# Kernel tuning notes

Measured on AMD Instinct MI355X. Metric: run time of the kernel, lower is better.

## Reference

```python
import jax, jax.numpy as jnp
import numpy as np

D_MODEL = 512
D_ATTN = 128


def setup_inputs() -> dict:
    key = jax.random.key(0)
    k1, k2, k3, k4, k5 = jax.random.split(key, 5)
    B, N = 4, 4096
    x = jax.random.normal(k1, (B, N, D_MODEL), dtype=jnp.float32)
    key_mask = jnp.ones((B, N, 1), dtype=jnp.float32)
    # nn.Linear params (stored as [in, out] for x @ W)
    W_qkv = jax.random.normal(k2, (D_MODEL, 3 * D_ATTN), dtype=jnp.float32) / np.sqrt(D_MODEL)
    b_qkv = jax.random.normal(k3, (3 * D_ATTN,), dtype=jnp.float32) * 0.01
    W_out = jax.random.normal(k4, (D_ATTN, D_MODEL), dtype=jnp.float32) / np.sqrt(D_ATTN)
    b_out = jax.random.normal(k5, (D_MODEL,), dtype=jnp.float32) * 0.01
    return {"x": x, "key_mask": key_mask, "W_qkv": W_qkv, "b_qkv": b_qkv,
            "W_out": W_out, "b_out": b_out}


def reference(x, key_mask, W_qkv, b_qkv, W_out, b_out):
    # Fused QKV projection: [B, N, 3*d_attn]
    qkv = jnp.einsum('bnd,de->bne', x, W_qkv) + b_qkv
    q, k, v = jnp.split(qkv, 3, axis=-1)  # each [B, N, d_attn]
    d_attn = q.shape[-1]
    scale = 1.0 / np.sqrt(d_attn)
    # Full [B, N, N] score matrix (faithful to original einsum)
    scores = jnp.einsum('bnd,bmd->bnm', q, k)
    # Causal mask applied BEFORE scaling (as in original: mask, then *scale)
    N = x.shape[1]
    causal = jnp.tril(jnp.ones((N, N), dtype=bool))  # True = keep
    scores = jnp.where(causal[None, :, :], scores, -jnp.inf)
    scores = scores * scale
    attn = jax.nn.softmax(scores, axis=-1)  # dropout is identity in eval
    out = jnp.einsum('bnm,bmd->bnd', attn, v)
    out = out * key_mask  # broadcast [B, N, 1]
    out = jnp.einsum('bnd,de->bne', out, W_out) + b_out
    return out
```

## Files before the change

### kernel.cpp

```cpp
#include <hip/hip_runtime.h>
#include <hip/hip_bf16.h>
#include <math.h>

typedef __attribute__((ext_vector_type(4))) float f32x4;
typedef __attribute__((ext_vector_type(4))) float fvec4;
typedef __attribute__((ext_vector_type(8))) short bf16x8_t;
typedef __attribute__((ext_vector_type(4))) short bf16x4_t;

static constexpr int BATCH = 4;
static constexpr int SEQ = 4096;
static constexpr int DM = 512;
static constexpr int DA = 128;
static constexpr int BN = BATCH * SEQ;
static constexpr int IPB = 187;
static constexpr int N_ITEMS = BATCH * IPB;

static constexpr float MASKV = -3.0e38f;
static constexpr float MINIT = -1.0e30f;

static __device__ __forceinline__ unsigned short f2bf(float f) {
  unsigned u = __builtin_bit_cast(unsigned, f);
  u += 0x7fffu + ((u >> 16) & 1u);
  return (unsigned short)(u >> 16);
}
static __device__ __forceinline__ float bf2f(unsigned short u) {
  return __builtin_bit_cast(float, ((unsigned)u) << 16);
}
static __device__ __forceinline__ float fexp2(float x) {
#if __has_builtin(__builtin_amdgcn_exp2f)
  return __builtin_amdgcn_exp2f(x);
#else
  return exp2f(x);
#endif
}
static __device__ __forceinline__ unsigned pkbf(float lo, float hi) {
  unsigned r;
  asm("v_cvt_pk_bf16_f32 %0, %1, %2" : "=v"(r) : "v"(lo), "v"(hi));
  return r;
}

#define GLDS16(gsrc, ldst)                                                        \
  __builtin_amdgcn_global_load_lds(                                               \
      (const __attribute__((address_space(1))) void*)(gsrc),                      \
      (__attribute__((address_space(3))) void*)(ldst), 16, 0, 0)

static constexpr float QSC = 0.08838834764831845f * 1.4426950408889634f;

__global__ __launch_bounds__(256) void prep_kernel(
    const float* __restrict__ x, const float* __restrict__ Wqkv,
    const float* __restrict__ Wout, unsigned short* __restrict__ xbf,
    unsigned short* __restrict__ WqT, unsigned short* __restrict__ WoT) {
  long long i = ((long long)blockIdx.x * 256 + threadIdx.x) * 8;
  if (i < (long long)BN * DM) {
    fvec4 a = *(const fvec4*)&x[i];
    fvec4 b = *(const fvec4*)&x[i + 4];
    union { bf16x8_t v; unsigned short u[8]; } pk;
    pk.u[0] = f2bf(a[0]); pk.u[1] = f2bf(a[1]); pk.u[2] = f2bf(a[2]); pk.u[3] = f2bf(a[3]);
    pk.u[4] = f2bf(b[0]); pk.u[5] = f2bf(b[1]); pk.u[6] = f2bf(b[2]); pk.u[7] = f2bf(b[3]);
    *(bf16x8_t*)&xbf[i] = pk.v;
  }
  int t = blockIdx.x * 256 + threadIdx.x;
  if (t < 512 * 384) {
    int k = t / 384, n = t - k * 384;
    WqT[n * 512 + k] = f2bf(Wqkv[t]);
  }
  if (t < 128 * 512) {
    int k = t >> 9, n = t & 511;
    WoT[n * 128 + k] = f2bf(Wout[t]);
  }
}

__global__ __launch_bounds__(512, 4) void qkv_kernel(
    const unsigned short* __restrict__ xbf, const unsigned short* __restrict__ WqT,
    const float* __restrict__ bias, unsigned short* __restrict__ qbf,
    unsigned short* __restrict__ kpk, unsigned short* __restrict__ vpk) {
  __shared__ unsigned short Alds[128 * 64];
  __shared__ unsigned short Blds[128 * 64];

  const int m0 = blockIdx.x * 128;
  const int n0 = blockIdx.y * 128;
  const int tid = threadIdx.x;
  const int wave = tid >> 6, lane = tid & 63;
  const int g = lane >> 4, lr = lane & 15;
  const int wm = wave >> 2, wn = wave & 3;

  const int srow = lane >> 3;
  const int sslot = lane & 7;
  const int sksw = ((sslot ^ srow) * 8);

  f32x4 acc[4][2] = {};

  for (int kb = 0; kb < DM; kb += 64) {
    __syncthreads();
#pragma unroll
    for (int i = 0; i < 2; ++i) {
      int ch = wave * 2 + i;
      GLDS16(&xbf[(size_t)(m0 + ch * 8 + srow) * DM + kb + sksw],
             (char*)Alds + ch * 1024);
      GLDS16(&WqT[(size_t)(n0 + ch * 8 + srow) * DM + kb + sksw],
             (char*)Blds + ch * 1024);
    }
    asm volatile("s_waitcnt vmcnt(0)" ::: "memory");
    __syncthreads();

#pragma unroll
    for (int c2 = 0; c2 < 2; ++c2) {
      bf16x8_t ar[4], br[2];
#pragma unroll
      for (int mi = 0; mi < 4; ++mi) {
        int row = wm * 64 + mi * 16 + lr;
        ar[mi] = *(const bf16x8_t*)&Alds[row * 64 + (((c2 * 4 + g) ^ (row & 7)) * 8)];
      }
#pragma unroll
      for (int ni = 0; ni < 2; ++ni) {
        int row = wn * 32 + ni * 16 + lr;
        br[ni] = *(const bf16x8_t*)&Blds[row * 64 + (((c2 * 4 + g) ^ (row & 7)) * 8)];
      }
#pragma unroll
      for (int mi = 0; mi < 4; ++mi)
#pragma unroll
        for (int ni = 0; ni < 2; ++ni)
          acc[mi][ni] = __builtin_amdgcn_mfma_f32_16x16x32_bf16(ar[mi], br[ni],
                                                                acc[mi][ni], 0, 0, 0);
    }
  }

  if (n0 == 0) {
#pragma unroll
    for (int ni = 0; ni < 2; ++ni) {
      int col = wn * 32 + ni * 16 + lr;
      float bv = bias[col];
#pragma unroll
      for (int mi = 0; mi < 4; ++mi) {
        int tokb = m0 + wm * 64 + mi * 16 + 4 * g;
#pragma unroll
        for (int r = 0; r < 4; ++r)
          qbf[(size_t)(tokb + r) * DA + col] = f2bf((acc[mi][ni][r] + bv) * QSC);
      }
    }
  } else if (n0 == 128) {
#pragma unroll
    for (int ni = 0; ni < 2; ++ni) {
      int kd = wn * 32 + ni * 16 + lr;
      float bv = bias[128 + kd];
      int unit = (kd >> 5) * 4 + ((kd >> 3) & 3);
      int elem = kd & 7;
#pragma unroll
      for (int mi = 0; mi < 4; ++mi) {
        int tokb = m0 + wm * 64 + mi * 16 + 4 * g;
#pragma unroll
        for (int r = 0; r < 4; ++r) {
          int token = tokb + r;
          int tile32 = token >> 5;
          int u = (((token >> 4) & 1) * 16) + unit;
          kpk[(size_t)tile32 * 4096 + u * 128 + (token & 15) * 8 + elem] =
              f2bf(acc[mi][ni][r] + bv);
        }
      }
    }
  } else {
#pragma unroll
    for (int mi = 0; mi < 4; ++mi) {
      int keyb = m0 + wm * 64 + mi * 16 + 4 * g;
      int tile32 = keyb >> 5;
      int kl0 = keyb & 31;
      int gp = (kl0 >> 2) & 3;
      int jhi = kl0 >> 4;
#pragma unroll
      for (int ni = 0; ni < 2; ++ni) {
        int d = wn * 32 + ni * 16 + lr;
        float bv = bias[256 + d];
        union { bf16x4_t v; unsigned short u[4]; } pk;
#pragma unroll
        for (int r = 0; r < 4; ++r) pk.u[r] = f2bf(acc[mi][ni][r] + bv);
        int unit = (d >> 4) * 4 + gp;
        *(bf16x4_t*)&vpk[(size_t)tile32 * 4096 + unit * 128 + (d & 15) * 8 + jhi * 4] =
            pk.v;
      }
    }
  }
}

static __device__ __forceinline__ void softmax64(
    f32x4 s[4], float& m_r, float& l_r, f32x4* oacc, bf16x8_t pb[2]) {
  float tmax = MASKV;
#pragma unroll
  for (int ct = 0; ct < 4; ++ct)
#pragma unroll
    for (int r = 0; r < 4; ++r) tmax = fmaxf(tmax, s[ct][r]);
  tmax = fmaxf(tmax, __shfl_xor(tmax, 16, 64));
  tmax = fmaxf(tmax, __shfl_xor(tmax, 32, 64));
  if (!__all(tmax <= m_r + 10.0f)) {
    float mn = fmaxf(m_r, tmax);
    float al = fexp2(m_r - mn);
    m_r = mn;
    l_r *= al;
#pragma unroll
    for (int t = 0; t < 8; ++t)
#pragma unroll
      for (int r = 0; r < 4; ++r) oacc[t][r] *= al;
  }
  float rs = 0.f;
#pragma unroll
  for (int ct = 0; ct < 4; ++ct)
#pragma unroll
    for (int r = 0; r < 4; ++r) {
      float p = fexp2(s[ct][r] - m_r);
      s[ct][r] = p;
      rs += p;
    }
  rs += __shfl_xor(rs, 16, 64);
  rs += __shfl_xor(rs, 32, 64);
  l_r += rs;
#pragma unroll
  for (int h = 0; h < 2; ++h) {
    union { unsigned u[4]; bf16x8_t v; } pk;
    pk.u[0] = pkbf(s[2 * h][0], s[2 * h][1]);
    pk.u[1] = pkbf(s[2 * h][2], s[2 * h][3]);
    pk.u[2] = pkbf(s[2 * h + 1][0], s[2 * h + 1][1]);
    pk.u[3] = pkbf(s[2 * h + 1][2], s[2 * h + 1][3]);
    pb[h] = pk.v;
  }
}

__global__ __launch_bounds__(256, 3) void attn_kernel(
    const unsigned short* __restrict__ qbf, const unsigned short* __restrict__ kpk,
    const unsigned short* __restrict__ vpk, const float* __restrict__ key_mask,
    unsigned short* __restrict__ part_o, float* __restrict__ part_ml,
    unsigned short* __restrict__ ctx) {
  __shared__ unsigned short Klds[2][8192];
  __shared__ unsigned short Vlds[8192];

  const int flat = blockIdx.x;
  const int b = flat & 3;
  const int idxr = flat >> 2;
  int rem = idxr;
  int qb = 31;
  for (;;) {
    int nc = (qb + 3) / 3;
    if (rem < nc) break;
    rem -= nc;
    --qb;
  }
  const int ci = rem;
  const bool direct = (qb < 3);
  const int key0 = ci * 384;
  const int nkeys = min(384, (qb + 1) * 128 - key0);
  const int nt = nkeys >> 6;

  const int tid = threadIdx.x;
  const int wave = tid >> 6, lane = tid & 63;
  const int g = lane >> 4, lr = lane & 15;
  const int q0 = wave * 16 + lr;
  const int q1 = q0 + 64;

  bf16x8_t qf0[4], qf1[4];
  {
    const unsigned short* qbase = qbf + ((size_t)(b * SEQ + qb * 128)) * DA + g * 8;
#pragma unroll
    for (int c = 0; c < 4; ++c) {
      qf0[c] = *(const bf16x8_t*)(qbase + (size_t)q0 * DA + c * 32);
      qf1[c] = *(const bf16x8_t*)(qbase + (size_t)q1 * DA + c * 32);
    }
  }

  f32x4 oacc0[8] = {}, oacc1[8] = {};
  float m0r = MINIT, l0 = 0.f, m1r = MINIT, l1 = 0.f;

  const int t32b = b * 128 + ci * 12;
  const unsigned short* ksrc = kpk + (size_t)t32b * 4096 + wave * 2048 + lane * 8;
  const unsigned short* vsrc = vpk + (size_t)t32b * 4096 + wave * 2048 + lane * 8;

#define STAGEK(buf, tt)                                                      \
  do {                                                                       \
    char* kd_ = (char*)Klds[buf] + wave * 4096;                              \
    _Pragma("unroll")                                                        \
    for (int i_ = 0; i_ < 4; ++i_)                                           \
      GLDS16(ksrc + (size_t)(tt) * 8192 + i_ * 512, kd_ + i_ * 1024);        \
  } while (0)
#define STAGEV(tt)                                                           \
  do {                                                                       \
    char* vd_ = (char*)Vlds + wave * 4096;                                   \
    _Pragma("unroll")                                                        \
    for (int i_ = 0; i_ < 4; ++i_)                                           \
      GLDS16(vsrc + (size_t)(tt) * 8192 + i_ * 512, vd_ + i_ * 1024);        \
  } while (0)

  STAGEK(0, 0);

  for (int tt = 0; tt < nt; ++tt) {
    const int cur = tt & 1;
    STAGEV(tt);
    if (tt + 1 < nt) {
      STAGEK(cur ^ 1, tt + 1);
      asm volatile("s_waitcnt vmcnt(8)" ::: "memory");
    } else {
      asm volatile("s_waitcnt vmcnt(4)" ::: "memory");
    }
    __builtin_amdgcn_s_barrier();
    __builtin_amdgcn_sched_barrier(0);

    f32x4 s0[4] = {}, s1[4] = {};
    __builtin_amdgcn_s_setprio(1);
#pragma unroll
    for (int ct = 0; ct < 4; ++ct)
#pragma unroll
      for (int c = 0; c < 4; ++c) {
        bf16x8_t kf = *(const bf16x8_t*)&Klds[cur][(ct >> 1) * 4096 +
                                                   (((ct & 1) * 16 + c * 4 + g) * 16 + lr) * 8];
        s0[ct] = __builtin_amdgcn_mfma_f32_16x16x32_bf16(kf, qf0[c], s0[ct], 0, 0, 0);
        s1[ct] = __builtin_amdgcn_mfma_f32_16x16x32_bf16(kf, qf1[c], s1[ct], 0, 0, 0);
      }
    __builtin_amdgcn_s_setprio(0);

    const int koff = key0 + tt * 64 - qb * 128;
    if (koff + 63 > wave * 16) {
      int thr = q0 - koff;
#pragma unroll
      for (int ct = 0; ct < 4; ++ct)
#pragma unroll
        for (int r = 0; r < 4; ++r)
          if (16 * ct + 4 * g + r > thr) s0[ct][r] = MASKV;
    }
    if (koff + 63 > 64 + wave * 16) {
      int thr = q1 - koff;
#pragma unroll
      for (int ct = 0; ct < 4; ++ct)
#pragma unroll
        for (int r = 0; r < 4; ++r)
          if (16 * ct + 4 * g + r > thr) s1[ct][r] = MASKV;
    }

    bf16x8_t pb0[2], pb1[2];
    softmax64(s0, m0r, l0, oacc0, pb0);
    softmax64(s1, m1r, l1, oacc1, pb1);

    if (tt + 1 < nt) {
      asm volatile("s_waitcnt vmcnt(4)" ::: "memory");
    } else {
      asm volatile("s_waitcnt vmcnt(0)" ::: "memory");
    }
    __builtin_amdgcn_s_barrier();
    __builtin_amdgcn_sched_barrier(0);

    __builtin_amdgcn_s_setprio(1);
#pragma unroll
    for (int t = 0; t < 8; ++t)
#pragma unroll
      for (int h = 0; h < 2; ++h) {
        bf16x8_t vf = *(const bf16x8_t*)&Vlds[h * 4096 + ((t * 4 + g) * 16 + lr) * 8];
        oacc0[t] = __builtin_amdgcn_mfma_f32_16x16x32_bf16(vf, pb0[h], oacc0[t], 0, 0, 0);
        oacc1[t] = __builtin_amdgcn_mfma_f32_16x16x32_bf16(vf, pb1[h], oacc1[t], 0, 0, 0);
      }
    __builtin_amdgcn_s_setprio(0);

    __builtin_amdgcn_s_barrier();
  }
#undef STAGEK
#undef STAGEV

  const int slot = b * IPB + idxr;
#pragma unroll
  for (int grp = 0; grp < 2; ++grp) {
    const int row = grp ? q1 : q0;
    const f32x4* oa = grp ? oacc1 : oacc0;
    const float mr = grp ? m1r : m0r;
    const float lr_ = grp ? l1 : l0;
    if (direct) {
      float km = key_mask[b * SEQ + qb * 128 + row];
      float inv = km / lr_;
      unsigned short* co = ctx + ((size_t)(b * SEQ + qb * 128 + row)) * DA;
#pragma unroll
      for (int t = 0; t < 8; ++t) {
        union { bf16x4_t v; unsigned short u[4]; } pk;
#pragma unroll
        for (int r = 0; r < 4; ++r) pk.u[r] = f2bf(oa[t][r] * inv);
        *(bf16x4_t*)&co[t * 16 + 4 * g] = pk.v;
      }
    } else {
      unsigned short* po = part_o + (size_t)slot * 16384 + (size_t)row * 128;
#pragma unroll
      for (int t = 0; t < 8; ++t) {
        union { bf16x4_t v; unsigned short u[4]; } pk;
#pragma unroll
        for (int r = 0; r < 4; ++r) pk.u[r] = f2bf(oa[t][r]);
        *(bf16x4_t*)&po[t * 16 + 4 * g] = pk.v;
      }
      if (g == 0) {
        float2 ml = make_float2(mr, lr_);
        *(float2*)&part_ml[((size_t)slot * 128 + row) * 2] = ml;
      }
    }
  }
}

__global__ __launch_bounds__(512) void combine_kernel(
    const unsigned short* __restrict__ part_o, const float* __restrict__ part_ml,
    const float* __restrict__ key_mask, unsigned short* __restrict__ ctx) {
  const int qb = 3 + (blockIdx.x >> 2);
  const int rq = blockIdx.x & 3;
  const int b = blockIdx.y;
  const int nc = (qb + 3) / 3;
  int idx0 = 0;
  for (int q = 31; q > qb; --q) idx0 += (q + 3) / 3;
  const int row = rq * 32 + (threadIdx.x >> 4);
  const int cs = threadIdx.x & 15;

  float m = MINIT;
  for (int ci = 0; ci < nc; ++ci) {
    int slot = b * IPB + idx0 + ci;
    m = fmaxf(m, part_ml[((size_t)slot * 128 + row) * 2 + 0]);
  }
  float l = 0.f;
  float acc[8];
#pragma unroll
  for (int k = 0; k < 8; ++k) acc[k] = 0.f;
  for (int ci = 0; ci < nc; ++ci) {
    int slot = b * IPB + idx0 + ci;
    float mi = part_ml[((size_t)slot * 128 + row) * 2 + 0];
    float li = part_ml[((size_t)slot * 128 + row) * 2 + 1];
    float w = fexp2(mi - m);
    l += w * li;
    const unsigned short* po =
        part_o + (size_t)slot * 16384 + (size_t)row * 128 + cs * 8;
    bf16x8_t v = *(const bf16x8_t*)po;
#pragma unroll
    for (int jj = 0; jj < 8; ++jj) acc[jj] += w * bf2f((unsigned short)v[jj]);
  }
  int rowg = b * SEQ + qb * 128 + row;
  float sc = key_mask[rowg] / l;
  union { bf16x8_t v; unsigned short u[8]; } pk;
#pragma unroll
  for (int jj = 0; jj < 8; ++jj) pk.u[jj] = f2bf(acc[jj] * sc);
  *(bf16x8_t*)&ctx[(size_t)rowg * 128 + cs * 8] = pk.v;
}

__global__ __launch_bounds__(512, 4) void outproj_kernel(
    const unsigned short* __restrict__ ctx, const unsigned short* __restrict__ WoT,
    const float* __restrict__ bias, float* __restrict__ out) {
  __shared__ unsigned short Alds[128 * 64];
  __shared__ unsigned short Blds[128 * 64];

  const int m0 = blockIdx.x * 128;
  const int n0 = blockIdx.y * 128;
  const int tid = threadIdx.x;
  const int wave = tid >> 6, lane = tid & 63;
  const int g = lane >> 4, lr = lane & 15;
  const int wm = wave >> 2, wn = wave & 3;

  const int srow = lane >> 3;
  const int sslot = lane & 7;
  const int sksw = ((sslot ^ srow) * 8);

  f32x4 acc[4][2] = {};

  for (int kb = 0; kb < DA; kb += 64) {
    __syncthreads();
#pragma unroll
    for (int i = 0; i < 2; ++i) {
      int ch = wave * 2 + i;
      GLDS16(&ctx[(size_t)(m0 + ch * 8 + srow) * DA + kb + sksw],
             (char*)Alds + ch * 1024);
      GLDS16(&WoT[(size_t)(n0 + ch * 8 + srow) * DA + kb + sksw],
             (char*)Blds + ch * 1024);
    }
    asm volatile("s_waitcnt vmcnt(0)" ::: "memory");
    __syncthreads();

#pragma unroll
    for (int c2 = 0; c2 < 2; ++c2) {
      bf16x8_t ar[4], br[2];
#pragma unroll
      for (int mi = 0; mi < 4; ++mi) {
        int row = wm * 64 + mi * 16 + lr;
        ar[mi] = *(const bf16x8_t*)&Alds[row * 64 + (((c2 * 4 + g) ^ (row & 7)) * 8)];
      }
#pragma unroll
      for (int ni = 0; ni < 2; ++ni) {
        int row = wn * 32 + ni * 16 + lr;
        br[ni] = *(const bf16x8_t*)&Blds[row * 64 + (((c2 * 4 + g) ^ (row & 7)) * 8)];
      }
#pragma unroll
      for (int mi = 0; mi < 4; ++mi)
#pragma unroll
        for (int ni = 0; ni < 2; ++ni)
          acc[mi][ni] = __builtin_amdgcn_mfma_f32_16x16x32_bf16(ar[mi], br[ni],
                                                                acc[mi][ni], 0, 0, 0);
    }
  }

#pragma unroll
  for (int ni = 0; ni < 2; ++ni) {
    int col = n0 + wn * 32 + ni * 16 + lr;
    float bv = bias[col];
#pragma unroll
    for (int mi = 0; mi < 4; ++mi) {
      int tokb = m0 + wm * 64 + mi * 16 + 4 * g;
#pragma unroll
      for (int r = 0; r < 4; ++r)
        out[(size_t)(tokb + r) * DM + col] = acc[mi][ni][r] + bv;
    }
  }
}

extern "C" void kernel_launch(void* const* d_in, const int* in_sizes, int n_in,
                              void* d_out, int out_size, void* d_ws, size_t ws_size,
                              hipStream_t stream) {
  const float* x = (const float*)d_in[0];
  const float* key_mask = (const float*)d_in[1];
  const float* W_qkv = (const float*)d_in[2];
  const float* b_qkv = (const float*)d_in[3];
  const float* W_out = (const float*)d_in[4];
  const float* b_out = (const float*)d_in[5];
  float* out = (float*)d_out;

  unsigned short* ws = (unsigned short*)d_ws;
  unsigned short* qbf = ws;
  unsigned short* kpk = qbf + (size_t)BN * DA;
  unsigned short* vpk = kpk + (size_t)BN * DA;
  unsigned short* ctx = vpk + (size_t)BN * DA;
  unsigned short* xbf = ctx + (size_t)BN * DA;
  unsigned short* WqT = xbf + (size_t)BN * DM;
  unsigned short* WoT = WqT + (size_t)384 * 512;
  unsigned short* part_o = WoT + (size_t)512 * 128;
  float* part_ml = (float*)(part_o + (size_t)N_ITEMS * 16384);

  prep_kernel<<<dim3((BN * DM / 8 + 255) / 256), 256, 0, stream>>>(
      x, W_qkv, W_out, xbf, WqT, WoT);
  qkv_kernel<<<dim3(BN / 128, 3), 512, 0, stream>>>(xbf, WqT, b_qkv, qbf, kpk, vpk);
  attn_kernel<<<dim3(N_ITEMS), 256, 0, stream>>>(qbf, kpk, vpk, key_mask,
                                                 part_o, part_ml, ctx);
  combine_kernel<<<dim3(29 * 4, 4), 512, 0, stream>>>(part_o, part_ml, key_mask, ctx);
  outproj_kernel<<<dim3(BN / 128, 4), 512, 0, stream>>>(ctx, WoT, b_out, out);
}
```

Measured before the change: 75.54 us.

## Prefetch K/V tiles into registers instead of direct global-to-LDS loads

Replaces the double-buffered direct global-to-LDS K staging and the separate V staging with register prefetch. Each iteration writes the previously loaded K/V tile from registers into a single LDS buffer and then issues global loads for the next tile. The per-iteration barrier count drops from three to two, and K LDS use is halved, which could help occupancy. In exchange it needs extra VGPRs for the prefetch registers, and the wait for the global loads now falls on the next iteration's LDS store rather than being overlapped through async LDS loads.

```diff
diff --git a/kernel.cpp b/kernel.cpp
--- a/kernel.cpp
+++ b/kernel.cpp
@@ -228,7 +228,7 @@
     const unsigned short* __restrict__ vpk, const float* __restrict__ key_mask,
     unsigned short* __restrict__ part_o, float* __restrict__ part_ml,
     unsigned short* __restrict__ ctx) {
-  __shared__ unsigned short Klds[2][8192];
+  __shared__ unsigned short Klds[8192];
   __shared__ unsigned short Vlds[8192];
 
   const int flat = blockIdx.x;
@@ -270,32 +270,32 @@
   const int t32b = b * 128 + ci * 12;
   const unsigned short* ksrc = kpk + (size_t)t32b * 4096 + wave * 2048 + lane * 8;
   const unsigned short* vsrc = vpk + (size_t)t32b * 4096 + wave * 2048 + lane * 8;
-
-#define STAGEK(buf, tt)                                                      \
+  char* kdst = (char*)Klds + wave * 4096 + (lane << 4);
+  char* vdst = (char*)Vlds + wave * 4096 + (lane << 4);
+
+  bf16x8_t kf_[4], vf_[4];
+#define LOADR(tt)                                                            \
   do {                                                                       \
-    char* kd_ = (char*)Klds[buf] + wave * 4096;                              \
     _Pragma("unroll")                                                        \
-    for (int i_ = 0; i_ < 4; ++i_)                                           \
-      GLDS16(ksrc + (size_t)(tt) * 8192 + i_ * 512, kd_ + i_ * 1024);        \
+    for (int i_ = 0; i_ < 4; ++i_) {                                         \
+      kf_[i_] = *(const bf16x8_t*)(ksrc + (size_t)(tt) * 8192 + i_ * 512);   \
+      vf_[i_] = *(const bf16x8_t*)(vsrc + (size_t)(tt) * 8192 + i_ * 512);   \
+    }                                                                        \
   } while (0)
-#define STAGEV(tt)                                                           \
-  do {                                                                       \
-    char* vd_ = (char*)Vlds + wave * 4096;                                   \
-    _Pragma("unroll")                                                        \
-    for (int i_ = 0; i_ < 4; ++i_)                                           \
-      GLDS16(vsrc + (size_t)(tt) * 8192 + i_ * 512, vd_ + i_ * 1024);        \
-  } while (0)
-
-  STAGEK(0, 0);
+
+  LOADR(0);
 
   for (int tt = 0; tt < nt; ++tt) {
-    const int cur = tt & 1;
-    STAGEV(tt);
-    if (tt + 1 < nt) {
-      STAGEK(cur ^ 1, tt + 1);
-      asm volatile("s_waitcnt vmcnt(8)" ::: "memory");
-    } else {
-      asm volatile("s_waitcnt vmcnt(4)" ::: "memory");
+    __builtin_amdgcn_s_barrier();
+#pragma unroll
+    for (int i_ = 0; i_ < 4; ++i_) {
+      *(bf16x8_t*)(kdst + i_ * 1024) = kf_[i_];
+      *(bf16x8_t*)(vdst + i_ * 1024) = vf_[i_];
+    }
+    asm volatile("s_waitcnt lgkmcnt(0)" ::: "memory");
+    {
+      int tn = (tt + 1 < nt) ? tt + 1 : tt;
+      LOADR(tn);
     }
     __builtin_amdgcn_s_barrier();
     __builtin_amdgcn_sched_barrier(0);
@@ -306,8 +306,8 @@
     for (int ct = 0; ct < 4; ++ct)
 #pragma unroll
       for (int c = 0; c < 4; ++c) {
-        bf16x8_t kf = *(const bf16x8_t*)&Klds[cur][(ct >> 1) * 4096 +
-                                                   (((ct & 1) * 16 + c * 4 + g) * 16 + lr) * 8];
+        bf16x8_t kf = *(const bf16x8_t*)&Klds[(ct >> 1) * 4096 +
+                                              (((ct & 1) * 16 + c * 4 + g) * 16 + lr) * 8];
         s0[ct] = __builtin_amdgcn_mfma_f32_16x16x32_bf16(kf, qf0[c], s0[ct], 0, 0, 0);
         s1[ct] = __builtin_amdgcn_mfma_f32_16x16x32_bf16(kf, qf1[c], s1[ct], 0, 0, 0);
       }
@@ -334,14 +334,6 @@
     bf16x8_t pb0[2], pb1[2];
     softmax64(s0, m0r, l0, oacc0, pb0);
     softmax64(s1, m1r, l1, oacc1, pb1);
-
-    if (tt + 1 < nt) {
-      asm volatile("s_waitcnt vmcnt(4)" ::: "memory");
-    } else {
-      asm volatile("s_waitcnt vmcnt(0)" ::: "memory");
-    }
-    __builtin_amdgcn_s_barrier();
-    __builtin_amdgcn_sched_barrier(0);
 
     __builtin_amdgcn_s_setprio(1);
 #pragma unroll
@@ -353,11 +345,8 @@
         oacc1[t] = __builtin_amdgcn_mfma_f32_16x16x32_bf16(vf, pb1[h], oacc1[t], 0, 0, 0);
       }
     __builtin_amdgcn_s_setprio(0);
-
-    __builtin_amdgcn_s_barrier();
-  }
-#undef STAGEK
-#undef STAGEV
+  }
+#undef LOADR
 
   const int slot = b * IPB + idxr;
 #pragma unroll
```

Result: slower. 84.43 us (+11.8%).

## Fuse x fp32-to-bf16 conversion into QKV GEMM tile loading

Applied to the files above, without the earlier changes.

Removes the standalone conversion pass that wrote a bf16 copy of x, and instead loads fp32 x tiles directly in the QKV GEMM. It converts them with packed bf16 instructions and stores them into the swizzled LDS layout. The weight transpose/convert kernel is shrunk to a smaller grid. This eliminates one full read/write pass over the activation, at the cost of reading fp32 x (twice the bytes) once per output column block. It also replaces async global-to-LDS loads for A with register-staged loads.

```diff
diff --git a/kernel.cpp b/kernel.cpp
--- a/kernel.cpp
+++ b/kernel.cpp
@@ -46,19 +46,9 @@
 
 static constexpr float QSC = 0.08838834764831845f * 1.4426950408889634f;
 
-__global__ __launch_bounds__(256) void prep_kernel(
-    const float* __restrict__ x, const float* __restrict__ Wqkv,
-    const float* __restrict__ Wout, unsigned short* __restrict__ xbf,
+__global__ __launch_bounds__(256) void prep_w_kernel(
+    const float* __restrict__ Wqkv, const float* __restrict__ Wout,
     unsigned short* __restrict__ WqT, unsigned short* __restrict__ WoT) {
-  long long i = ((long long)blockIdx.x * 256 + threadIdx.x) * 8;
-  if (i < (long long)BN * DM) {
-    fvec4 a = *(const fvec4*)&x[i];
-    fvec4 b = *(const fvec4*)&x[i + 4];
-    union { bf16x8_t v; unsigned short u[8]; } pk;
-    pk.u[0] = f2bf(a[0]); pk.u[1] = f2bf(a[1]); pk.u[2] = f2bf(a[2]); pk.u[3] = f2bf(a[3]);
-    pk.u[4] = f2bf(b[0]); pk.u[5] = f2bf(b[1]); pk.u[6] = f2bf(b[2]); pk.u[7] = f2bf(b[3]);
-    *(bf16x8_t*)&xbf[i] = pk.v;
-  }
   int t = blockIdx.x * 256 + threadIdx.x;
   if (t < 512 * 384) {
     int k = t / 384, n = t - k * 384;
@@ -71,7 +61,7 @@
 }
 
 __global__ __launch_bounds__(512, 4) void qkv_kernel(
-    const unsigned short* __restrict__ xbf, const unsigned short* __restrict__ WqT,
+    const float* __restrict__ x, const unsigned short* __restrict__ WqT,
     const float* __restrict__ bias, unsigned short* __restrict__ qbf,
     unsigned short* __restrict__ kpk, unsigned short* __restrict__ vpk) {
   __shared__ unsigned short Alds[128 * 64];
@@ -95,10 +85,26 @@
 #pragma unroll
     for (int i = 0; i < 2; ++i) {
       int ch = wave * 2 + i;
-      GLDS16(&xbf[(size_t)(m0 + ch * 8 + srow) * DM + kb + sksw],
-             (char*)Alds + ch * 1024);
       GLDS16(&WqT[(size_t)(n0 + ch * 8 + srow) * DM + kb + sksw],
              (char*)Blds + ch * 1024);
+    }
+    fvec4 af32[2][2];
+#pragma unroll
+    for (int i = 0; i < 2; ++i) {
+      int ch = wave * 2 + i;
+      const float* ap = &x[(size_t)(m0 + ch * 8 + srow) * DM + kb + sksw];
+      af32[i][0] = *(const fvec4*)ap;
+      af32[i][1] = *(const fvec4*)(ap + 4);
+    }
+#pragma unroll
+    for (int i = 0; i < 2; ++i) {
+      int ch = wave * 2 + i;
+      union { unsigned u[4]; bf16x8_t v; } pk;
+      pk.u[0] = pkbf(af32[i][0][0], af32[i][0][1]);
+      pk.u[1] = pkbf(af32[i][0][2], af32[i][0][3]);
+      pk.u[2] = pkbf(af32[i][1][0], af32[i][1][1]);
+      pk.u[3] = pkbf(af32[i][1][2], af32[i][1][3]);
+      *(bf16x8_t*)&Alds[ch * 512 + lane * 8] = pk.v;
     }
     asm volatile("s_waitcnt vmcnt(0)" ::: "memory");
     __syncthreads();
@@ -525,9 +531,8 @@
   unsigned short* part_o = WoT + (size_t)512 * 128;
   float* part_ml = (float*)(part_o + (size_t)N_ITEMS * 16384);
 
-  prep_kernel<<<dim3((BN * DM / 8 + 255) / 256), 256, 0, stream>>>(
-      x, W_qkv, W_out, xbf, WqT, WoT);
-  qkv_kernel<<<dim3(BN / 128, 3), 512, 0, stream>>>(xbf, WqT, b_qkv, qbf, kpk, vpk);
+  prep_w_kernel<<<dim3(768), 256, 0, stream>>>(W_qkv, W_out, WqT, WoT);
+  qkv_kernel<<<dim3(BN / 128, 3), 512, 0, stream>>>(x, WqT, b_qkv, qbf, kpk, vpk);
   attn_kernel<<<dim3(N_ITEMS), 256, 0, stream>>>(qbf, kpk, vpk, key_mask,
                                                  part_o, part_ml, ctx);
   combine_kernel<<<dim3(29 * 4, 4), 512, 0, stream>>>(part_o, part_ml, key_mask, ctx);
```

After: 72.85 us, median of 3. 1.04x faster.
